# Performance work log

Measured on AMD Instinct MI355X. Metric: run time of the kernel, lower is better.

## Reference

```python
import jax, jax.numpy as jnp
import numpy as np

DIM = 768
NUM_HEADS = 12
HEAD_DIM = DIM // NUM_HEADS
SCALE = HEAD_DIM ** -0.5


def setup_inputs() -> dict:
    key = jax.random.key(0)
    k1, k2, k3, k4, k5 = jax.random.split(key, 5)
    B, N = 8, 2048
    x = jax.random.normal(k1, (B, N, DIM), dtype=jnp.float32)
    mask = jax.random.randint(k2, (B, N), 0, 2, dtype=jnp.int32)
    # ensure at least one valid key per batch row to avoid all -inf softmax rows
    mask = mask.at[:, 0].set(1)
    w_qkv = jax.random.normal(k3, (DIM, 3 * DIM), dtype=jnp.float32) * (DIM ** -0.5)
    w_proj = jax.random.normal(k4, (DIM, DIM), dtype=jnp.float32) * (DIM ** -0.5)
    b_proj = jax.random.normal(k5, (DIM,), dtype=jnp.float32) * 0.02
    return {"x": x, "mask": mask, "w_qkv": w_qkv, "w_proj": w_proj, "b_proj": b_proj}


def reference(x, mask, w_qkv, w_proj, b_proj):
    B, N, C = x.shape
    qkv = (x @ w_qkv).reshape(B, N, 3, NUM_HEADS, HEAD_DIM)
    qkv = jnp.transpose(qkv, (2, 0, 3, 1, 4))  # [3, B, H, N, D]
    q, k, v = qkv[0], qkv[1], qkv[2]
    q = q * SCALE
    # fp32 upcast for scores (inputs already fp32; explicit for fidelity)
    attn = jnp.einsum('bhqd,bhkd->bhqk', q.astype(jnp.float32), k.astype(jnp.float32))
    key_mask = mask.astype(bool)[:, None, None, :]  # [B,1,1,N]
    attn = jnp.where(key_mask, attn, -jnp.inf)
    attn = jax.nn.softmax(attn, axis=-1).astype(x.dtype)
    out = jnp.einsum('bhqk,bhkd->bhqd', attn, v)  # [B,H,N,D]
    out = jnp.transpose(out, (0, 2, 1, 3)).reshape(B, N, C)
    return out @ w_proj + b_proj
```

## Files before the change

### kernel.cpp

```cpp
#include <hip/hip_runtime.h>
#include <hip/hip_bf16.h>
#include <stdint.h>

#define NHEAD 12
#define SEQ   2048
#define NB    8
#define MTOK  (NB*SEQ)
#define DIMC  768
#define QKVN  (3*DIMC)

typedef __attribute__((ext_vector_type(8))) short bf16x8;
typedef __attribute__((ext_vector_type(4))) float f32x4;
typedef __attribute__((ext_vector_type(16))) float f32x16;
typedef __attribute__((ext_vector_type(4))) unsigned short u16x4;
typedef __attribute__((ext_vector_type(4))) unsigned int u32x4;

typedef const __attribute__((address_space(1))) char glb_char;
typedef __attribute__((address_space(3))) char lds_char;

__device__ __forceinline__ unsigned short f2bf(float f) {
  union { float f; unsigned u; } v; v.f = f;
  return (unsigned short)((v.u + 0x7FFFu + ((v.u >> 16) & 1u)) >> 16);
}

__device__ __forceinline__ void gload_lds16(const void* g, void* l) {
  __builtin_amdgcn_global_load_lds((glb_char*)g, (lds_char*)l, 16, 0, 0);
}

__device__ __forceinline__ unsigned cvtpk_bf16(float lo, float hi) {
  unsigned d;
  asm("v_cvt_pk_bf16_f32 %0, %1, %2" : "=v"(d) : "v"(lo), "v"(hi));
  return d;
}

#define QSCALE 0.18033688011112042f
#define MASKBIAS -30000.0f

__global__ void __launch_bounds__(256, 8)
cvt_bf16_kernel(const float* __restrict__ in,
                unsigned short* __restrict__ out, int n4) {
  int idx = blockIdx.x * blockDim.x + threadIdx.x;
  int stride = gridDim.x * blockDim.x;
  for (int i = idx; i < n4; i += stride) {
    float4 v = ((const float4*)in)[i];
    u16x4 o;
    o.x = f2bf(v.x); o.y = f2bf(v.y); o.z = f2bf(v.z); o.w = f2bf(v.w);
    ((u16x4*)out)[i] = o;
  }
}

__global__ void __launch_bounds__(256, 4)
maskscan_kernel(const int* __restrict__ mask, int* __restrict__ posmap,
                float* __restrict__ mbias_c, int* __restrict__ nvalid) {
  __shared__ int sums[256];
  __shared__ int btot;
  const int b = blockIdx.x, t = threadIdx.x;
  const int* m = mask + b * SEQ;
  int loc[8];
  int s = 0;
  #pragma unroll
  for (int i = 0; i < 8; i++) { loc[i] = (m[t * 8 + i] != 0) ? 1 : 0; s += loc[i]; }
  sums[t] = s;
  __syncthreads();
  for (int off = 1; off < 256; off <<= 1) {
    int v = (t >= off) ? sums[t - off] : 0;
    __syncthreads();
    sums[t] += v;
    __syncthreads();
  }
  int excl = sums[t] - s;
  if (t == 255) btot = sums[255];
  __syncthreads();
  const int nv = btot;
  #pragma unroll
  for (int i = 0; i < 8; i++) {
    posmap[b * SEQ + t * 8 + i] = loc[i] ? excl : -1;
    excl += loc[i];
  }
  for (int j = t; j < SEQ; j += 256)
    mbias_c[b * SEQ + j] = (j < nv) ? 0.0f : MASKBIAS;
  if (t == 0) nvalid[b] = nv;
}

__global__ void __launch_bounds__(256, 8)
zerotail_kernel(unsigned short* __restrict__ kc, unsigned short* __restrict__ vc,
                const int* __restrict__ nvalid) {
  const int bh = blockIdx.x, t = threadIdx.x;
  const int b = bh / NHEAD;
  const int nv = nvalid[b];
  const int pad = (nv + 63) & ~63;
  const int nz = pad - nv;
  if (nz == 0) return;
  unsigned short* kcb = kc + (size_t)bh * SEQ * 64;
  unsigned short* vcb = vc + (size_t)bh * 64 * SEQ;
  for (int i = t; i < nz * 64; i += 256) {
    int r = i >> 6, d = i & 63;
    kcb[(nv + r) * 64 + d] = 0;
  }
  for (int i = t; i < 64 * nz; i += 256) {
    int d = i / nz, c = i - d * nz;
    vcb[(size_t)d * SEQ + nv + c] = 0;
  }
}

__global__ void __launch_bounds__(256, 8)
transpose_cvt_kernel(const float* __restrict__ in,
                     unsigned short* __restrict__ out,
                     int R, int C) {
  __shared__ float tile[32][33];
  int c0 = blockIdx.x * 32, r0 = blockIdx.y * 32;
  int tx = threadIdx.x & 31, ty = threadIdx.x >> 5;
  #pragma unroll
  for (int i = 0; i < 32; i += 8)
    tile[ty + i][tx] = in[(size_t)(r0 + ty + i) * C + c0 + tx];
  __syncthreads();
  #pragma unroll
  for (int i = 0; i < 32; i += 8)
    out[(size_t)(c0 + ty + i) * R + r0 + tx] = f2bf(tile[tx][ty + i]);
}

__global__ void __launch_bounds__(256, 2)
qkv_gemm_kernel(const unsigned short* __restrict__ xb,
                const unsigned short* __restrict__ wT,
                unsigned short* __restrict__ qo,
                unsigned short* __restrict__ ko,
                unsigned short* __restrict__ vto,
                const int* __restrict__ posmap) {
  __shared__ short lA[128 * 32];
  __shared__ short lB[128 * 32];
  const int t = threadIdx.x;
  const int lane = t & 63, w = t >> 6;
  const int m0 = blockIdx.x * 128;
  const int n0 = blockIdx.y * 128;
  const int wr = (w >> 1) * 64, wc = (w & 1) * 64;
  const int l15 = lane & 15, lg = lane >> 4;
  const int sr = t >> 2;
  const int sc = t & 3;

  f32x4 acc[4][4] = {};

  for (int k0 = 0; k0 < DIMC; k0 += 32) {
    __syncthreads();
    #pragma unroll
    for (int i = 0; i < 2; i++) {
      int row = i * 64 + sr;
      int cb = (sc ^ ((row >> 1) & 3)) * 8;
      gload_lds16(xb + (size_t)(m0 + row) * DIMC + k0 + cb,
                  (char*)lA + i * 4096 + w * 1024);
      gload_lds16(wT + (size_t)(n0 + row) * DIMC + k0 + cb,
                  (char*)lB + i * 4096 + w * 1024);
    }
    __syncthreads();
    bf16x8 af[4], bfr[4];
    #pragma unroll
    for (int mi = 0; mi < 4; mi++) {
      int m = wr + mi * 16 + l15;
      af[mi] = *(const bf16x8*)&lA[m * 32 + ((lg ^ ((m >> 1) & 3)) << 3)];
    }
    #pragma unroll
    for (int nj = 0; nj < 4; nj++) {
      int n = wc + nj * 16 + l15;
      bfr[nj] = *(const bf16x8*)&lB[n * 32 + ((lg ^ ((n >> 1) & 3)) << 3)];
    }
    #pragma unroll
    for (int mi = 0; mi < 4; mi++)
      #pragma unroll
      for (int nj = 0; nj < 4; nj++)
        acc[mi][nj] = __builtin_amdgcn_mfma_f32_16x16x32_bf16(af[mi], bfr[nj], acc[mi][nj], 0, 0, 0);
  }

  #pragma unroll
  for (int mi = 0; mi < 4; mi++) {
    int tok0 = m0 + wr + mi * 16 + 4 * lg;
    int bb = tok0 >> 11;
    int nn0 = tok0 & 2047;
    int pm[4];
    #pragma unroll
    for (int r = 0; r < 4; r++) pm[r] = posmap[tok0 + r];
    #pragma unroll
    for (int nj = 0; nj < 4; nj++) {
      int col = n0 + wc + nj * 16 + l15;
      int which = col / DIMC;
      int ch = col - which * DIMC;
      int hh = ch >> 6, dd = ch & 63;
      size_t hb = (size_t)(bb * NHEAD + hh);
      if (which == 0) {
        size_t base = (hb * SEQ + nn0) * 64 + dd;
        #pragma unroll
        for (int r = 0; r < 4; r++)
          qo[base + (size_t)r * 64] = f2bf(acc[mi][nj][r] * QSCALE);
      } else if (which == 1) {
        #pragma unroll
        for (int r = 0; r < 4; r++)
          if (pm[r] >= 0)
            ko[(hb * SEQ + pm[r]) * 64 + dd] = f2bf(acc[mi][nj][r]);
      } else {
        #pragma unroll
        for (int r = 0; r < 4; r++)
          if (pm[r] >= 0)
            vto[(hb * 64 + dd) * SEQ + pm[r]] = f2bf(acc[mi][nj][r]);
      }
    }
  }
}

__global__ void __launch_bounds__(256, 4)
attn_kernel(const unsigned short* __restrict__ qbuf,
            const unsigned short* __restrict__ kbuf,
            const unsigned short* __restrict__ vtbuf,
            const float* __restrict__ mbias_c,
            const int* __restrict__ nvalid,
            unsigned short* __restrict__ ao) {
  __shared__ short lKV[2][8192];
  __shared__ float lmask[2][64];
  const int t = threadIdx.x, lane = t & 63, w = t >> 6;
  const int l31 = lane & 31, hi = lane >> 5;
  const int bid = blockIdx.x;
  const int qt = bid / 96;
  const int bh = bid - qt * 96;
  const int b = bh / NHEAD, h = bh - b * NHEAD;
  const int q0 = qt * 128 + w * 32;
  const unsigned short* qb = qbuf + (size_t)bh * SEQ * 64;
  const unsigned short* kb = kbuf + (size_t)bh * SEQ * 64;
  const unsigned short* vb = vtbuf + (size_t)bh * 64 * SEQ;
  const float* mb = mbias_c + b * SEQ;
  const int ntiles = (nvalid[b] + 63) >> 6;

  auto STAGE = [&](int tile, int bsel) {
    int kv0 = tile * 64;
    #pragma unroll
    for (int i = 0; i < 2; i++) {
      int c = i * 4 + w;
      gload_lds16(kb + (size_t)(kv0 + lane) * 64 + c * 8,
                  (char*)lKV + bsel * 16384 + c * 1024);
      gload_lds16(vb + (size_t)lane * SEQ + kv0 + c * 8,
                  (char*)lKV + bsel * 16384 + 8192 + c * 1024);
    }
    if (w == 0)
      __builtin_amdgcn_global_load_lds((glb_char*)(mb + tile * 64 + lane),
                                       (lds_char*)&lmask[bsel][0], 4, 0, 0);
  };

  bf16x8 qf[4];
  #pragma unroll
  for (int dblk = 0; dblk < 4; dblk++)
    qf[dblk] = *(const bf16x8*)(qb + (size_t)(q0 + l31) * 64 + dblk * 16 + hi * 8);

  f32x16 O[2] = {};
  float ls[4] = {0.f, 0.f, 0.f, 0.f};

  STAGE(0, 0);
  __syncthreads();

  for (int it = 0; it < ntiles; ++it) {
    const int bsel = it & 1;
    const short* Kb = &lKV[bsel][0];
    const short* Vb = &lKV[bsel][4096];
    if (it + 1 < ntiles) STAGE(it + 1, bsel ^ 1);

    #pragma unroll
    for (int kb2 = 0; kb2 < 2; kb2++) {
      f32x4 mb4[4];
      #pragma unroll
      for (int g = 0; g < 4; g++)
        mb4[g] = *(const f32x4*)&lmask[bsel][kb2 * 32 + g * 8 + hi * 4];
      f32x16 S;
      #pragma unroll
      for (int r = 0; r < 16; r++) S[r] = mb4[r >> 2][r & 3];

      __builtin_amdgcn_s_setprio(1);
      #pragma unroll
      for (int dblk = 0; dblk < 4; dblk++) {
        bf16x8 kf = *(const bf16x8*)&Kb[(dblk * 2 + hi) * 512 + (kb2 * 32 + l31) * 8];
        S = __builtin_amdgcn_mfma_f32_32x32x16_bf16(kf, qf[dblk], S, 0, 0, 0);
      }
      __builtin_amdgcn_s_setprio(0);

      float p[16];
      #pragma unroll
      for (int r = 0; r < 16; r++) p[r] = __builtin_amdgcn_exp2f(S[r]);
      #pragma unroll
      for (int r = 0; r < 16; r++) ls[r & 3] += p[r];

      #pragma unroll
      for (int half = 0; half < 2; half++) {
        unsigned a0 = cvtpk_bf16(p[half * 8 + 0], p[half * 8 + 1]);
        unsigned a1 = cvtpk_bf16(p[half * 8 + 2], p[half * 8 + 3]);
        unsigned a2 = cvtpk_bf16(p[half * 8 + 4], p[half * 8 + 5]);
        unsigned a3 = cvtpk_bf16(p[half * 8 + 6], p[half * 8 + 7]);
        asm("v_permlane32_swap_b32 %0, %1" : "+v"(a0), "+v"(a2));
        asm("v_permlane32_swap_b32 %0, %1" : "+v"(a1), "+v"(a3));
        union { u32x4 u; bf16x8 f; } cv;
        cv.u = (u32x4){a0, a1, a2, a3};
        __builtin_amdgcn_s_setprio(1);
        #pragma unroll
        for (int dt = 0; dt < 2; dt++) {
          bf16x8 vf = *(const bf16x8*)&Vb[(kb2 * 4 + half * 2 + hi) * 512 + (dt * 32 + l31) * 8];
          O[dt] = __builtin_amdgcn_mfma_f32_32x32x16_bf16(cv.f, vf, O[dt], 0, 0, 0);
        }
        __builtin_amdgcn_s_setprio(0);
      }
    }

    if (it + 1 < ntiles) {
      asm volatile("s_waitcnt vmcnt(0)" ::: "memory");
      __builtin_amdgcn_s_barrier();
    }
  }

  float* lrs = (float*)&lKV[0][0];
  float tot = (ls[0] + ls[1]) + (ls[2] + ls[3]);
  tot += __shfl_xor(tot, 32);
  lrs[w * 32 + l31] = tot;

  float inv[16];
  #pragma unroll
  for (int r = 0; r < 16; r++)
    inv[r] = 1.0f / lrs[w * 32 + (r & 3) + 8 * (r >> 2) + 4 * hi];

  #pragma unroll
  for (int dt = 0; dt < 2; dt++) {
    #pragma unroll
    for (int r = 0; r < 16; r++) {
      int qrow = q0 + (r & 3) + 8 * (r >> 2) + 4 * hi;
      size_t base = ((size_t)(b * SEQ + qrow)) * DIMC + h * 64 + dt * 32 + l31;
      ao[base] = __bfloat16_as_ushort(__float2bfloat16(O[dt][r] * inv[r]));
    }
  }
}

__global__ void __launch_bounds__(256, 2)
proj_gemm_kernel(const unsigned short* __restrict__ ab,
                 const unsigned short* __restrict__ wT,
                 const float* __restrict__ bias,
                 float* __restrict__ out) {
  __shared__ short lA[128 * 32];
  __shared__ short lB[128 * 32];
  const int t = threadIdx.x;
  const int lane = t & 63, w = t >> 6;
  const int m0 = blockIdx.x * 128;
  const int n0 = blockIdx.y * 128;
  const int wr = (w >> 1) * 64, wc = (w & 1) * 64;
  const int l15 = lane & 15, lg = lane >> 4;
  const int sr = t >> 2;
  const int sc = t & 3;

  f32x4 acc[4][4] = {};

  for (int k0 = 0; k0 < DIMC; k0 += 32) {
    __syncthreads();
    #pragma unroll
    for (int i = 0; i < 2; i++) {
      int row = i * 64 + sr;
      int cb = (sc ^ ((row >> 1) & 3)) * 8;
      gload_lds16(ab + (size_t)(m0 + row) * DIMC + k0 + cb,
                  (char*)lA + i * 4096 + w * 1024);
      gload_lds16(wT + (size_t)(n0 + row) * DIMC + k0 + cb,
                  (char*)lB + i * 4096 + w * 1024);
    }
    __syncthreads();
    bf16x8 af[4], bfr[4];
    #pragma unroll
    for (int mi = 0; mi < 4; mi++) {
      int m = wr + mi * 16 + l15;
      af[mi] = *(const bf16x8*)&lA[m * 32 + ((lg ^ ((m >> 1) & 3)) << 3)];
    }
    #pragma unroll
    for (int nj = 0; nj < 4; nj++) {
      int n = wc + nj * 16 + l15;
      bfr[nj] = *(const bf16x8*)&lB[n * 32 + ((lg ^ ((n >> 1) & 3)) << 3)];
    }
    #pragma unroll
    for (int mi = 0; mi < 4; mi++)
      #pragma unroll
      for (int nj = 0; nj < 4; nj++)
        acc[mi][nj] = __builtin_amdgcn_mfma_f32_16x16x32_bf16(af[mi], bfr[nj], acc[mi][nj], 0, 0, 0);
  }

  #pragma unroll
  for (int mi = 0; mi < 4; mi++) {
    int row0 = m0 + wr + mi * 16 + 4 * lg;
    #pragma unroll
    for (int nj = 0; nj < 4; nj++) {
      int col = n0 + wc + nj * 16 + l15;
      float bv = bias[col];
      #pragma unroll
      for (int r = 0; r < 4; r++)
        out[(size_t)(row0 + r) * DIMC + col] = acc[mi][nj][r] + bv;
    }
  }
}

extern "C" void kernel_launch(void* const* d_in, const int* in_sizes, int n_in,
                              void* d_out, int out_size, void* d_ws, size_t ws_size,
                              hipStream_t stream) {
  const float* x      = (const float*)d_in[0];
  const int*   mask   = (const int*)d_in[1];
  const float* w_qkv  = (const float*)d_in[2];
  const float* w_proj = (const float*)d_in[3];
  const float* b_proj = (const float*)d_in[4];
  float* out = (float*)d_out;

  unsigned short* ws = (unsigned short*)d_ws;
  unsigned short* xb     = ws;
  unsigned short* wqkvT  = xb    + (size_t)MTOK * DIMC;
  unsigned short* wprojT = wqkvT + (size_t)QKVN * DIMC;
  unsigned short* qbuf   = wprojT + (size_t)DIMC * DIMC;
  unsigned short* kbuf   = qbuf  + (size_t)MTOK * DIMC;
  unsigned short* vtbuf  = kbuf  + (size_t)MTOK * DIMC;
  float*          mbias_c = (float*)(vtbuf + (size_t)MTOK * DIMC);
  int*            posmap  = (int*)(mbias_c + MTOK);
  int*            nvalid  = posmap + MTOK;
  unsigned short* aob    = xb;

  cvt_bf16_kernel<<<2048, 256, 0, stream>>>(x, xb, MTOK * DIMC / 4);
  maskscan_kernel<<<NB, 256, 0, stream>>>(mask, posmap, mbias_c, nvalid);
  transpose_cvt_kernel<<<dim3(QKVN / 32, DIMC / 32), 256, 0, stream>>>(w_qkv, wqkvT, DIMC, QKVN);
  transpose_cvt_kernel<<<dim3(DIMC / 32, DIMC / 32), 256, 0, stream>>>(w_proj, wprojT, DIMC, DIMC);
  qkv_gemm_kernel<<<dim3(128, 18), 256, 0, stream>>>(xb, wqkvT, qbuf, kbuf, vtbuf, posmap);
  zerotail_kernel<<<NB * NHEAD, 256, 0, stream>>>(kbuf, vtbuf, nvalid);
  attn_kernel<<<1536, 256, 0, stream>>>(qbuf, kbuf, vtbuf, mbias_c, nvalid, aob);
  proj_gemm_kernel<<<dim3(128, 6), 256, 0, stream>>>(aob, wprojT, b_proj, out);
}
```

Before: 217.8 us.

## Double-buffer LDS tiles in QKV and projection GEMMs to overlap loads

Both GEMM kernels now keep two LDS buffers and issue the global-to-LDS loads for the next K-slice before running the MFMAs on the current one. This replaces two barriers per iteration with one waitcnt plus barrier, so global load latency can hide behind compute. The MFMA block is also wrapped in s_setprio to favour math waves. LDS per block doubles to 32KB, which could affect occupancy at 2 blocks per CU. Correctness relies on the single barrier also ordering LDS reads of the old buffer before it is overwritten two iterations later.

```diff
diff --git a/kernel.cpp b/kernel.cpp
--- a/kernel.cpp
+++ b/kernel.cpp
@@ -126,8 +126,8 @@
                 unsigned short* __restrict__ ko,
                 unsigned short* __restrict__ vto,
                 const int* __restrict__ posmap) {
-  __shared__ short lA[128 * 32];
-  __shared__ short lB[128 * 32];
+  __shared__ short lA[2][128 * 32];
+  __shared__ short lB[2][128 * 32];
   const int t = threadIdx.x;
   const int lane = t & 63, w = t >> 6;
   const int m0 = blockIdx.x * 128;
@@ -137,36 +137,53 @@
   const int sr = t >> 2;
   const int sc = t & 3;
 
-  f32x4 acc[4][4] = {};
-
-  for (int k0 = 0; k0 < DIMC; k0 += 32) {
-    __syncthreads();
+  auto STAGE = [&](int k0, int bsel) {
     #pragma unroll
     for (int i = 0; i < 2; i++) {
       int row = i * 64 + sr;
       int cb = (sc ^ ((row >> 1) & 3)) * 8;
       gload_lds16(xb + (size_t)(m0 + row) * DIMC + k0 + cb,
-                  (char*)lA + i * 4096 + w * 1024);
+                  (char*)lA + bsel * 8192 + i * 4096 + w * 1024);
       gload_lds16(wT + (size_t)(n0 + row) * DIMC + k0 + cb,
-                  (char*)lB + i * 4096 + w * 1024);
-    }
-    __syncthreads();
+                  (char*)lB + bsel * 8192 + i * 4096 + w * 1024);
+    }
+  };
+
+  f32x4 acc[4][4] = {};
+
+  STAGE(0, 0);
+  asm volatile("s_waitcnt vmcnt(0)" ::: "memory");
+  __builtin_amdgcn_s_barrier();
+
+  for (int k0 = 0; k0 < DIMC; k0 += 32) {
+    const int bsel = (k0 >> 5) & 1;
+    if (k0 + 32 < DIMC) STAGE(k0 + 32, bsel ^ 1);
+    const short* A = &lA[bsel][0];
+    const short* B = &lB[bsel][0];
+
     bf16x8 af[4], bfr[4];
     #pragma unroll
     for (int mi = 0; mi < 4; mi++) {
       int m = wr + mi * 16 + l15;
-      af[mi] = *(const bf16x8*)&lA[m * 32 + ((lg ^ ((m >> 1) & 3)) << 3)];
+      af[mi] = *(const bf16x8*)&A[m * 32 + ((lg ^ ((m >> 1) & 3)) << 3)];
     }
     #pragma unroll
     for (int nj = 0; nj < 4; nj++) {
       int n = wc + nj * 16 + l15;
-      bfr[nj] = *(const bf16x8*)&lB[n * 32 + ((lg ^ ((n >> 1) & 3)) << 3)];
-    }
+      bfr[nj] = *(const bf16x8*)&B[n * 32 + ((lg ^ ((n >> 1) & 3)) << 3)];
+    }
+    __builtin_amdgcn_s_setprio(1);
     #pragma unroll
     for (int mi = 0; mi < 4; mi++)
       #pragma unroll
       for (int nj = 0; nj < 4; nj++)
         acc[mi][nj] = __builtin_amdgcn_mfma_f32_16x16x32_bf16(af[mi], bfr[nj], acc[mi][nj], 0, 0, 0);
+    __builtin_amdgcn_s_setprio(0);
+
+    if (k0 + 32 < DIMC) {
+      asm volatile("s_waitcnt vmcnt(0)" ::: "memory");
+      __builtin_amdgcn_s_barrier();
+    }
   }
 
   #pragma unroll
@@ -334,8 +351,8 @@
                  const unsigned short* __restrict__ wT,
                  const float* __restrict__ bias,
                  float* __restrict__ out) {
-  __shared__ short lA[128 * 32];
-  __shared__ short lB[128 * 32];
+  __shared__ short lA[2][128 * 32];
+  __shared__ short lB[2][128 * 32];
   const int t = threadIdx.x;
   const int lane = t & 63, w = t >> 6;
   const int m0 = blockIdx.x * 128;
@@ -345,36 +362,53 @@
   const int sr = t >> 2;
   const int sc = t & 3;
 
-  f32x4 acc[4][4] = {};
-
-  for (int k0 = 0; k0 < DIMC; k0 += 32) {
-    __syncthreads();
+  auto STAGE = [&](int k0, int bsel) {
     #pragma unroll
     for (int i = 0; i < 2; i++) {
       int row = i * 64 + sr;
       int cb = (sc ^ ((row >> 1) & 3)) * 8;
       gload_lds16(ab + (size_t)(m0 + row) * DIMC + k0 + cb,
-                  (char*)lA + i * 4096 + w * 1024);
+                  (char*)lA + bsel * 8192 + i * 4096 + w * 1024);
       gload_lds16(wT + (size_t)(n0 + row) * DIMC + k0 + cb,
-                  (char*)lB + i * 4096 + w * 1024);
-    }
-    __syncthreads();
+                  (char*)lB + bsel * 8192 + i * 4096 + w * 1024);
+    }
+  };
+
+  f32x4 acc[4][4] = {};
+
+  STAGE(0, 0);
+  asm volatile("s_waitcnt vmcnt(0)" ::: "memory");
+  __builtin_amdgcn_s_barrier();
+
+  for (int k0 = 0; k0 < DIMC; k0 += 32) {
+    const int bsel = (k0 >> 5) & 1;
+    if (k0 + 32 < DIMC) STAGE(k0 + 32, bsel ^ 1);
+    const short* A = &lA[bsel][0];
+    const short* B = &lB[bsel][0];
+
     bf16x8 af[4], bfr[4];
     #pragma unroll
     for (int mi = 0; mi < 4; mi++) {
       int m = wr + mi * 16 + l15;
-      af[mi] = *(const bf16x8*)&lA[m * 32 + ((lg ^ ((m >> 1) & 3)) << 3)];
+      af[mi] = *(const bf16x8*)&A[m * 32 + ((lg ^ ((m >> 1) & 3)) << 3)];
     }
     #pragma unroll
     for (int nj = 0; nj < 4; nj++) {
       int n = wc + nj * 16 + l15;
-      bfr[nj] = *(const bf16x8*)&lB[n * 32 + ((lg ^ ((n >> 1) & 3)) << 3)];
-    }
+      bfr[nj] = *(const bf16x8*)&B[n * 32 + ((lg ^ ((n >> 1) & 3)) << 3)];
+    }
+    __builtin_amdgcn_s_setprio(1);
     #pragma unroll
     for (int mi = 0; mi < 4; mi++)
       #pragma unroll
       for (int nj = 0; nj < 4; nj++)
         acc[mi][nj] = __builtin_amdgcn_mfma_f32_16x16x32_bf16(af[mi], bfr[nj], acc[mi][nj], 0, 0, 0);
+    __builtin_amdgcn_s_setprio(0);
+
+    if (k0 + 32 < DIMC) {
+      asm volatile("s_waitcnt vmcnt(0)" ::: "memory");
+      __builtin_amdgcn_s_barrier();
+    }
   }
 
   #pragma unroll
```

Result: no change. 218.9 us (+0.5%).
